# Optimization experiments

Hardware: AMD Instinct MI355X
Metric: run time of the kernel (lower is better)

Reference implementation:

```python
import jax, jax.numpy as jnp
import numpy as np

B, C_IN, C_OUT, E, H, W = 64, 384, 384, 8, 28, 28


def setup_inputs() -> dict:
    key = jax.random.key(0)
    k1, k2, k3 = jax.random.split(key, 3)
    x = jax.random.normal(k1, (B, C_IN, H, W), dtype=jnp.float32)
    routing_weights = jax.random.uniform(k2, (B, E), dtype=jnp.float32)
    # kaiming_normal_(mode='fan_out') per expert: std = sqrt(2 / fan_out), fan_out = out_channels * 1 * 1
    std = float(np.sqrt(2.0 / C_OUT))
    weight = jax.random.normal(k3, (E, C_OUT, C_IN), dtype=jnp.float32) * std
    return {"x": x, "routing_weights": routing_weights, "weight": weight}


def reference(x, routing_weights, weight):
    # Per-sample aggregated 1x1 conv weights: [b, c_out, c_in]
    agg = jnp.einsum('be,eoi->boi', routing_weights, weight)
    # Per-sample channel mixing (1x1 conv with groups=b == batched GEMM)
    out = jnp.einsum('boi,bihw->bohw', agg, x)
    return out
```

## Files before the change

### kernel.cpp

```cpp
#include <hip/hip_runtime.h>
#include <cstdint>

#define B_   64
#define CI_  384
#define CO_  384
#define HW_  784
#define E_   8
#define G_   (CI_ / 8)

typedef unsigned short ushort_t;
typedef unsigned int   uint_t;

typedef __attribute__((ext_vector_type(8))) short bf16x8;
typedef __attribute__((ext_vector_type(4))) float f32x4;

__device__ __forceinline__ ushort_t f2bf_rne(float f) {
  uint_t u = __builtin_bit_cast(uint_t, f);
  u += 0x7fffu + ((u >> 16) & 1u);
  return (ushort_t)(u >> 16);
}

__device__ __forceinline__ uint_t pack_bf16_trunc(float f0, float f1) {
  return __builtin_amdgcn_perm(__builtin_bit_cast(uint_t, f1),
                               __builtin_bit_cast(uint_t, f0),
                               0x07060302u);
}

#define AGG_BLOCKS 288
#define XQ_BLOCKS  (G_ * B_)

__global__ __launch_bounds__(256) void prep(const float* __restrict__ rw,
                                            const float* __restrict__ w,
                                            const float* __restrict__ x,
                                            ushort_t* __restrict__ agg,
                                            ushort_t* __restrict__ xq) {
  __shared__ float r[B_ * E_];
  const int blk = blockIdx.x;
  const int tid = threadIdx.x;

  if (blk < AGG_BLOCKS) {
    r[tid]       = rw[tid];
    r[tid + 256] = rw[tid + 256];
    const int base = blk * 512 + tid * 2;
    float2 wv[E_];
#pragma unroll
    for (int e = 0; e < E_; ++e)
      wv[e] = *(const float2*)&w[e * (CO_ * CI_) + base];
    __syncthreads();
#pragma unroll 8
    for (int b = 0; b < B_; ++b) {
      float ax = 0.f, ay = 0.f;
#pragma unroll
      for (int e = 0; e < E_; ++e) {
        const float rv = r[b * E_ + e];
        ax += rv * wv[e].x;
        ay += rv * wv[e].y;
      }
      const uint_t v = (uint_t)f2bf_rne(ax) | ((uint_t)f2bf_rne(ay) << 16);
      *(uint_t*)&agg[(size_t)b * (CO_ * CI_) + base] = v;
    }
  } else {
    const int idx = blk - AGG_BLOCKS;
    const int g = idx % G_;
    const int b = idx / G_;
    const float* xp = x + ((size_t)b * CI_ + g * 8) * HW_;
    ushort_t* op = xq + (((size_t)b * G_ + g) * HW_) * 8;
#pragma unroll
    for (int c = 0; c < 4; ++c) {
      const int hw = c * 256 + tid;
      if (hw < HW_) {
        float v[8];
#pragma unroll
        for (int j = 0; j < 8; ++j) v[j] = xp[(size_t)j * HW_ + hw];
        uint4 u;
        u.x = pack_bf16_trunc(v[0], v[1]);
        u.y = pack_bf16_trunc(v[2], v[3]);
        u.z = pack_bf16_trunc(v[4], v[5]);
        u.w = pack_bf16_trunc(v[6], v[7]);
        *(uint4*)&op[hw * 8] = u;
      }
    }
  }
}

#define BM 128
#define BN 128
#define BK 32
#define KIT (CI_ / BK)

__global__ __launch_bounds__(256, 3) void moe_gemm4(const ushort_t* __restrict__ Agg,
                                                    const ushort_t* __restrict__ Xq,
                                                    float* __restrict__ Out) {
  __shared__ __align__(16) ushort_t As[3][BM * BK];
  __shared__ __align__(16) ushort_t Bs[3][BN * BK];

  const int tid  = threadIdx.x;
  const int lane = tid & 63;
  const int wave = tid >> 6;
  const int wm = wave & 1, wn = wave >> 1;

  const int bx = blockIdx.x;
  const int by = blockIdx.y;
  const int bg  = by / 21;
  const int rem = by - bg * 21;
  const int mt  = rem / 7;
  const int nt  = rem - mt * 7;
  const int b   = bg * 8 + bx;

  const int sr0 = tid >> 2,          sq0 = (tid & 3) ^ ((tid >> 3) & 3);
  const int sr1 = (tid + 256) >> 2,  sq1 = (tid & 3) ^ (((tid + 256) >> 3) & 3);

  const ushort_t* Ab = Agg + (size_t)b * CO_ * CI_ + (size_t)(mt * BM) * CI_;
  const ushort_t* Asrc0 = Ab + sr0 * CI_ + sq0 * 8;
  const ushort_t* Asrc1 = Ab + sr1 * CI_ + sq1 * 8;

  int hw0 = nt * BN + sr0; hw0 = hw0 < HW_ ? hw0 : HW_ - 1;
  int hw1 = nt * BN + sr1; hw1 = hw1 < HW_ ? hw1 : HW_ - 1;
  const ushort_t* Xb = Xq + (size_t)b * G_ * HW_ * 8;
  const ushort_t* Bsrc0 = Xb + ((size_t)sq0 * HW_ + hw0) * 8;
  const ushort_t* Bsrc1 = Xb + ((size_t)sq1 * HW_ + hw1) * 8;

  const int l15 = lane & 15;
  const int lq  = lane >> 4;
  const int xqA = lq ^ ((l15 >> 1) & 3);

  f32x4 acc[4][4];
#pragma unroll
  for (int i = 0; i < 4; ++i)
#pragma unroll
    for (int j = 0; j < 4; ++j)
      acc[i][j] = (f32x4)0.f;

#define STAGE(PB, KK)                                                          \
  {                                                                            \
    __builtin_amdgcn_global_load_lds(                                          \
        (const __attribute__((address_space(1))) uint_t*)(Asrc0 + (KK) * BK),  \
        (__attribute__((address_space(3))) uint_t*)&As[PB][tid * 8], 16, 0, 0);\
    __builtin_amdgcn_global_load_lds(                                          \
        (const __attribute__((address_space(1))) uint_t*)(Asrc1 + (KK) * BK),  \
        (__attribute__((address_space(3))) uint_t*)&As[PB][(tid + 256) * 8],   \
        16, 0, 0);                                                             \
    const size_t bo_ = (size_t)(KK) * (4 * HW_ * 8);                           \
    __builtin_amdgcn_global_load_lds(                                          \
        (const __attribute__((address_space(1))) uint_t*)(Bsrc0 + bo_),        \
        (__attribute__((address_space(3))) uint_t*)&Bs[PB][tid * 8], 16, 0, 0);\
    __builtin_amdgcn_global_load_lds(                                          \
        (const __attribute__((address_space(1))) uint_t*)(Bsrc1 + bo_),        \
        (__attribute__((address_space(3))) uint_t*)&Bs[PB][(tid + 256) * 8],   \
        16, 0, 0);                                                             \
  }

#define COMPUTE(CB)                                                            \
  {                                                                            \
    bf16x8 a[4], bb[4];                                                        \
    _Pragma("unroll") for (int mf = 0; mf < 4; ++mf) {                         \
      const int row = wm * 64 + mf * 16 + l15;                                 \
      a[mf] = *(const bf16x8*)&As[CB][(row * 4 + xqA) * 8];                    \
    }                                                                          \
    _Pragma("unroll") for (int nf = 0; nf < 4; ++nf) {                         \
      const int col = wn * 64 + nf * 16 + l15;                                 \
      bb[nf] = *(const bf16x8*)&Bs[CB][(col * 4 + xqA) * 8];                   \
    }                                                                          \
    __builtin_amdgcn_s_setprio(1);                                             \
    _Pragma("unroll") for (int mf = 0; mf < 4; ++mf)                           \
      _Pragma("unroll") for (int nf = 0; nf < 4; ++nf)                         \
        acc[mf][nf] = __builtin_amdgcn_mfma_f32_16x16x32_bf16(a[mf], bb[nf],   \
                                                              acc[mf][nf],     \
                                                              0, 0, 0);        \
    __builtin_amdgcn_s_setprio(0);                                             \
  }

#define ITER_S(VM, CB, STG)                                                    \
  {                                                                            \
    asm volatile("s_waitcnt vmcnt(" #VM ")" ::: "memory");                     \
    __builtin_amdgcn_s_barrier();                                              \
    __builtin_amdgcn_sched_barrier(0);                                         \
    STAGE((STG) % 3, STG);                                                     \
    COMPUTE(CB);                                                               \
    __builtin_amdgcn_sched_barrier(0);                                         \
  }
#define ITER_N(VM, CB)                                                         \
  {                                                                            \
    asm volatile("s_waitcnt vmcnt(" #VM ")" ::: "memory");                     \
    __builtin_amdgcn_s_barrier();                                              \
    __builtin_amdgcn_sched_barrier(0);                                         \
    COMPUTE(CB);                                                               \
    __builtin_amdgcn_sched_barrier(0);                                         \
  }

  STAGE(0, 0);
  STAGE(1, 1);

#pragma unroll
  for (int t = 0; t < 10; ++t)
    ITER_S(4, t % 3, t + 2);

  ITER_N(4, 1);
  ITER_N(0, 2);

  float* Ob = Out + (size_t)b * CO_ * HW_;
#pragma unroll
  for (int mf = 0; mf < 4; ++mf) {
#pragma unroll
    for (int nf = 0; nf < 4; ++nf) {
      const int n = nt * BN + wn * 64 + nf * 16 + l15;
      if (n < HW_) {
        const int mbase = mt * BM + wm * 64 + mf * 16 + lq * 4;
#pragma unroll
        for (int r = 0; r < 4; ++r)
          Ob[(size_t)(mbase + r) * HW_ + n] = acc[mf][nf][r];
      }
    }
  }
}

extern "C" void kernel_launch(void* const* d_in, const int* in_sizes, int n_in,
                              void* d_out, int out_size, void* d_ws, size_t ws_size,
                              hipStream_t stream) {
  const float* x  = (const float*)d_in[0];
  const float* rw = (const float*)d_in[1];
  const float* w  = (const float*)d_in[2];
  float* out = (float*)d_out;

  ushort_t* agg = (ushort_t*)d_ws;
  ushort_t* xq  = agg + (size_t)B_ * CO_ * CI_;

  prep<<<AGG_BLOCKS + XQ_BLOCKS, 256, 0, stream>>>(rw, w, x, agg, xq);
  moe_gemm4<<<dim3(8, 21 * (B_ / 8)), 256, 0, stream>>>(agg, xq, out);
}
```

Measured before the change: 170.5 us.

## Fuse fp32-to-bf16 conversion of x into the GEMM's B-tile loading

The separate pass that converted x to a packed bf16 workspace is removed. The GEMM now reads fp32 x directly into registers, packs it to bf16 and writes it into swizzled LDS, double-buffered in registers alongside the async A loads. This drops a full write and re-read of the converted x through global memory. In exchange each x element is read as fp32 once per M tile (three times), the B path uses more VGPRs, and an extra LDS write and wait sit in every iteration.

```diff
diff --git a/kernel.cpp b/kernel.cpp
--- a/kernel.cpp
+++ b/kernel.cpp
@@ -6,7 +6,6 @@
 #define CO_  384
 #define HW_  784
 #define E_   8
-#define G_   (CI_ / 8)
 
 typedef unsigned short ushort_t;
 typedef unsigned int   uint_t;
@@ -27,59 +26,31 @@
 }
 
 #define AGG_BLOCKS 288
-#define XQ_BLOCKS  (G_ * B_)
-
-__global__ __launch_bounds__(256) void prep(const float* __restrict__ rw,
-                                            const float* __restrict__ w,
-                                            const float* __restrict__ x,
-                                            ushort_t* __restrict__ agg,
-                                            ushort_t* __restrict__ xq) {
+
+__global__ __launch_bounds__(256) void prep_agg(const float* __restrict__ rw,
+                                                const float* __restrict__ w,
+                                                ushort_t* __restrict__ agg) {
   __shared__ float r[B_ * E_];
-  const int blk = blockIdx.x;
   const int tid = threadIdx.x;
-
-  if (blk < AGG_BLOCKS) {
-    r[tid]       = rw[tid];
-    r[tid + 256] = rw[tid + 256];
-    const int base = blk * 512 + tid * 2;
-    float2 wv[E_];
-#pragma unroll
-    for (int e = 0; e < E_; ++e)
-      wv[e] = *(const float2*)&w[e * (CO_ * CI_) + base];
-    __syncthreads();
+  r[tid]       = rw[tid];
+  r[tid + 256] = rw[tid + 256];
+  const int base = blockIdx.x * 512 + tid * 2;
+  float2 wv[E_];
+#pragma unroll
+  for (int e = 0; e < E_; ++e)
+    wv[e] = *(const float2*)&w[e * (CO_ * CI_) + base];
+  __syncthreads();
 #pragma unroll 8
-    for (int b = 0; b < B_; ++b) {
-      float ax = 0.f, ay = 0.f;
-#pragma unroll
-      for (int e = 0; e < E_; ++e) {
-        const float rv = r[b * E_ + e];
-        ax += rv * wv[e].x;
-        ay += rv * wv[e].y;
-      }
-      const uint_t v = (uint_t)f2bf_rne(ax) | ((uint_t)f2bf_rne(ay) << 16);
-      *(uint_t*)&agg[(size_t)b * (CO_ * CI_) + base] = v;
+  for (int b = 0; b < B_; ++b) {
+    float ax = 0.f, ay = 0.f;
+#pragma unroll
+    for (int e = 0; e < E_; ++e) {
+      const float rv = r[b * E_ + e];
+      ax += rv * wv[e].x;
+      ay += rv * wv[e].y;
     }
-  } else {
-    const int idx = blk - AGG_BLOCKS;
-    const int g = idx % G_;
-    const int b = idx / G_;
-    const float* xp = x + ((size_t)b * CI_ + g * 8) * HW_;
-    ushort_t* op = xq + (((size_t)b * G_ + g) * HW_) * 8;
-#pragma unroll
-    for (int c = 0; c < 4; ++c) {
-      const int hw = c * 256 + tid;
-      if (hw < HW_) {
-        float v[8];
-#pragma unroll
-        for (int j = 0; j < 8; ++j) v[j] = xp[(size_t)j * HW_ + hw];
-        uint4 u;
-        u.x = pack_bf16_trunc(v[0], v[1]);
-        u.y = pack_bf16_trunc(v[2], v[3]);
-        u.z = pack_bf16_trunc(v[4], v[5]);
-        u.w = pack_bf16_trunc(v[6], v[7]);
-        *(uint4*)&op[hw * 8] = u;
-      }
-    }
+    const uint_t v = (uint_t)f2bf_rne(ax) | ((uint_t)f2bf_rne(ay) << 16);
+    *(uint_t*)&agg[(size_t)b * (CO_ * CI_) + base] = v;
   }
 }
 
@@ -88,8 +59,8 @@
 #define BK 32
 #define KIT (CI_ / BK)
 
-__global__ __launch_bounds__(256, 3) void moe_gemm4(const ushort_t* __restrict__ Agg,
-                                                    const ushort_t* __restrict__ Xq,
+__global__ __launch_bounds__(256, 3) void moe_gemm5(const float* __restrict__ X,
+                                                    const ushort_t* __restrict__ Agg,
                                                     float* __restrict__ Out) {
   __shared__ __align__(16) ushort_t As[3][BM * BK];
   __shared__ __align__(16) ushort_t Bs[3][BN * BK];
@@ -109,16 +80,18 @@
 
   const int sr0 = tid >> 2,          sq0 = (tid & 3) ^ ((tid >> 3) & 3);
   const int sr1 = (tid + 256) >> 2,  sq1 = (tid & 3) ^ (((tid + 256) >> 3) & 3);
-
   const ushort_t* Ab = Agg + (size_t)b * CO_ * CI_ + (size_t)(mt * BM) * CI_;
   const ushort_t* Asrc0 = Ab + sr0 * CI_ + sq0 * 8;
   const ushort_t* Asrc1 = Ab + sr1 * CI_ + sq1 * 8;
 
-  int hw0 = nt * BN + sr0; hw0 = hw0 < HW_ ? hw0 : HW_ - 1;
-  int hw1 = nt * BN + sr1; hw1 = hw1 < HW_ ? hw1 : HW_ - 1;
-  const ushort_t* Xb = Xq + (size_t)b * G_ * HW_ * 8;
-  const ushort_t* Bsrc0 = Xb + ((size_t)sq0 * HW_ + hw0) * 8;
-  const ushort_t* Bsrc1 = Xb + ((size_t)sq1 * HW_ + hw1) * 8;
+  const int n0  = (tid & 63) * 2;
+  const int khq = wave;
+  const int s0  = n0 * 4 + (khq ^ ((n0 >> 1) & 3));
+  const int bws0 = s0 * 8;
+  const int bws1 = bws0 + 32;
+  int gn0 = nt * BN + n0;
+  gn0 = gn0 > (HW_ - 2) ? (HW_ - 2) : gn0;
+  const float* XbCol = X + (size_t)b * CI_ * HW_ + (size_t)khq * 8 * HW_ + gn0;
 
   const int l15 = lane & 15;
   const int lq  = lane >> 4;
@@ -131,7 +104,9 @@
     for (int j = 0; j < 4; ++j)
       acc[i][j] = (f32x4)0.f;
 
-#define STAGE(PB, KK)                                                          \
+  float2 vA[8], vB[8];
+
+#define STAGE_A(PB, KK)                                                        \
   {                                                                            \
     __builtin_amdgcn_global_load_lds(                                          \
         (const __attribute__((address_space(1))) uint_t*)(Asrc0 + (KK) * BK),  \
@@ -140,14 +115,28 @@
         (const __attribute__((address_space(1))) uint_t*)(Asrc1 + (KK) * BK),  \
         (__attribute__((address_space(3))) uint_t*)&As[PB][(tid + 256) * 8],   \
         16, 0, 0);                                                             \
-    const size_t bo_ = (size_t)(KK) * (4 * HW_ * 8);                           \
-    __builtin_amdgcn_global_load_lds(                                          \
-        (const __attribute__((address_space(1))) uint_t*)(Bsrc0 + bo_),        \
-        (__attribute__((address_space(3))) uint_t*)&Bs[PB][tid * 8], 16, 0, 0);\
-    __builtin_amdgcn_global_load_lds(                                          \
-        (const __attribute__((address_space(1))) uint_t*)(Bsrc1 + bo_),        \
-        (__attribute__((address_space(3))) uint_t*)&Bs[PB][(tid + 256) * 8],   \
-        16, 0, 0);                                                             \
+  }
+
+#define LOADB(SET, KK)                                                         \
+  {                                                                            \
+    const float* p_ = XbCol + (size_t)((KK) * BK) * HW_;                       \
+    _Pragma("unroll") for (int j_ = 0; j_ < 8; ++j_)                           \
+        SET[j_] = *(const float2*)(p_ + (size_t)j_ * HW_);                     \
+  }
+
+#define PACKB(SET, PB)                                                         \
+  {                                                                            \
+    uint4 u0_, u1_;                                                            \
+    u0_.x = pack_bf16_trunc(SET[0].x, SET[1].x);                               \
+    u0_.y = pack_bf16_trunc(SET[2].x, SET[3].x);                               \
+    u0_.z = pack_bf16_trunc(SET[4].x, SET[5].x);                               \
+    u0_.w = pack_bf16_trunc(SET[6].x, SET[7].x);                               \
+    u1_.x = pack_bf16_trunc(SET[0].y, SET[1].y);                               \
+    u1_.y = pack_bf16_trunc(SET[2].y, SET[3].y);                               \
+    u1_.z = pack_bf16_trunc(SET[4].y, SET[5].y);                               \
+    u1_.w = pack_bf16_trunc(SET[6].y, SET[7].y);                               \
+    *(uint4*)&Bs[PB][bws0] = u0_;                                              \
+    *(uint4*)&Bs[PB][bws1] = u1_;                                              \
   }
 
 #define COMPUTE(CB)                                                            \
@@ -170,33 +159,37 @@
     __builtin_amdgcn_s_setprio(0);                                             \
   }
 
-#define ITER_S(VM, CB, STG)                                                    \
-  {                                                                            \
-    asm volatile("s_waitcnt vmcnt(" #VM ")" ::: "memory");                     \
+#define BODY(T, SET, VMSTR, STG_EN)                                            \
+  {                                                                            \
+    asm volatile("s_waitcnt vmcnt(" VMSTR ")" ::: "memory");                   \
+    __builtin_amdgcn_sched_barrier(0);                                         \
+    PACKB(SET, (T) % 3);                                                       \
+    asm volatile("s_waitcnt lgkmcnt(0)" ::: "memory");                         \
     __builtin_amdgcn_s_barrier();                                              \
     __builtin_amdgcn_sched_barrier(0);                                         \
-    STAGE((STG) % 3, STG);                                                     \
-    COMPUTE(CB);                                                               \
+    if (STG_EN) {                                                              \
+      STAGE_A(((T) + 2) % 3, (T) + 2);                                         \
+      LOADB(SET, (T) + 2);                                                     \
+    }                                                                          \
+    COMPUTE((T) % 3);                                                          \
     __builtin_amdgcn_sched_barrier(0);                                         \
   }
-#define ITER_N(VM, CB)                                                         \
-  {                                                                            \
-    asm volatile("s_waitcnt vmcnt(" #VM ")" ::: "memory");                     \
-    __builtin_amdgcn_s_barrier();                                              \
-    __builtin_amdgcn_sched_barrier(0);                                         \
-    COMPUTE(CB);                                                               \
-    __builtin_amdgcn_sched_barrier(0);                                         \
-  }
-
-  STAGE(0, 0);
-  STAGE(1, 1);
-
-#pragma unroll
-  for (int t = 0; t < 10; ++t)
-    ITER_S(4, t % 3, t + 2);
-
-  ITER_N(4, 1);
-  ITER_N(0, 2);
+
+  STAGE_A(0, 0); LOADB(vA, 0);
+  STAGE_A(1, 1); LOADB(vB, 1);
+
+  BODY(0, vA, "10", 1)
+  BODY(1, vB, "10", 1)
+  BODY(2, vA, "10", 1)
+  BODY(3, vB, "10", 1)
+  BODY(4, vA, "10", 1)
+  BODY(5, vB, "10", 1)
+  BODY(6, vA, "10", 1)
+  BODY(7, vB, "10", 1)
+  BODY(8, vA, "10", 1)
+  BODY(9, vB, "10", 1)
+  BODY(10, vA, "10", 0)
+  BODY(11, vB, "0", 0)
 
   float* Ob = Out + (size_t)b * CO_ * HW_;
 #pragma unroll
@@ -223,8 +216,7 @@
   float* out = (float*)d_out;
 
   ushort_t* agg = (ushort_t*)d_ws;
-  ushort_t* xq  = agg + (size_t)B_ * CO_ * CI_;
-
-  prep<<<AGG_BLOCKS + XQ_BLOCKS, 256, 0, stream>>>(rw, w, x, agg, xq);
-  moe_gemm4<<<dim3(8, 21 * (B_ / 8)), 256, 0, stream>>>(agg, xq, out);
-}
+
+  prep_agg<<<AGG_BLOCKS, 256, 0, stream>>>(rw, w, agg);
+  moe_gemm5<<<dim3(8, 21 * (B_ / 8)), 256, 0, stream>>>(x, agg, out);
+}
```

Result: slower. 180.7 us (+6.0%).
